# Kernel tuning notes

Hardware: AMD Instinct MI355X
Metric: run time of the kernel (lower is better)

The kernel has to match this reference:

```python
import jax, jax.numpy as jnp
import numpy as np

N_NODES = 100000
N_EDGES = 1600000
HIDDEN = 128


def setup_inputs() -> dict:
    key = jax.random.key(0)
    k1, k2, k3 = jax.random.split(key, 3)
    pos = jax.random.normal(k1, (N_NODES, 3), dtype=jnp.float32)
    edge_index = jax.random.randint(k2, (2, N_EDGES), 0, N_NODES, dtype=jnp.int64)
    vector_features = jax.random.normal(k3, (N_NODES, 3, HIDDEN), dtype=jnp.float32)
    return {"pos": pos, "edge_index": edge_index, "vector_features": vector_features}


def reference(pos, edge_index, vector_features):
    # pos: (N,3); edge_index: (2,E); vector_features: (N,3,H) (unused by original math)
    H = vector_features.shape[-1]
    n_nodes = pos.shape[0]
    row, col = edge_index[0], edge_index[1]

    edge_vec = pos[col] - pos[row]                                  # (E,3)
    edge_dist = jnp.linalg.norm(edge_vec, axis=-1, keepdims=True) + 1e-8
    unit_vec = edge_vec / edge_dist                                 # (E,3)

    # scatter-add of unit vectors to both endpoints
    direction_units = (jnp.zeros((n_nodes, 3), dtype=pos.dtype)
                       .at[row].add(unit_vec)
                       .at[col].add(-unit_vec))                     # (N,3)

    # sum over spatial dim of du*du -> squared norm, broadcast to hidden
    angular_info = jnp.broadcast_to(
        jnp.sum(direction_units * direction_units, axis=1, keepdims=True),
        (n_nodes, H))                                               # (N,H)

    # vectorized per-edge dihedral: project v_i, v_j off the edge direction
    v_i = direction_units[row]                                      # (E,3)
    v_j = direction_units[col]                                      # (E,3)
    dot_vi = jnp.sum(v_i * unit_vec, axis=-1, keepdims=True)
    dot_vj = jnp.sum(v_j * (-unit_vec), axis=-1, keepdims=True)
    w_ij = v_i - dot_vi * unit_vec
    w_ji = v_j - dot_vj * (-unit_vec)
    dihedral_val = jnp.sum(w_ij * w_ji, axis=-1, keepdims=True)     # (E,1)
    dihedral_info = jnp.broadcast_to(dihedral_val, (edge_index.shape[1], H))

    return (angular_info, dihedral_info, direction_units)
```

## Files before the change

kernel.cpp:

```cpp
#include <hip/hip_runtime.h>
#include <math.h>

#define N_NODES 100000
#define N_EDGES 1600000
#define HIDDEN 128

#define NBINS      256
#define BIN_NODES  391
#define BIN_CAP    16256
#define CUR_STRIDE 32
#define A_THREADS  1024
#define A_EPT      2
#define A_EPB      (A_THREADS * A_EPT)
#define A_BLOCKS   ((N_EDGES + A_EPB - 1) / A_EPB)
#define B_THREADS  1024

#define FP_SCALE   4194304.0f
#define FP_INV     (1.0f / 4194304.0f)


typedef float vfloat4 __attribute__((ext_vector_type(4)));

__global__ void zero_cursors_kernel(unsigned* __restrict__ cur) {
    cur[threadIdx.x * CUR_STRIDE] = 0u;
}

__global__ __launch_bounds__(A_THREADS) void bin_edges_kernel(
    const int* __restrict__ eidx,
    unsigned* __restrict__ cursors,
    unsigned* __restrict__ region)
{
    __shared__ unsigned cnt[NBINS];
    __shared__ unsigned base[NBINS];
    if (threadIdx.x < NBINS) cnt[threadIdx.x] = 0u;
    __syncthreads();

    const int e0 = blockIdx.x * A_EPB + threadIdx.x * 2;
    const bool valid = (e0 < N_EDGES);

    unsigned r[A_EPT], c[A_EPT], br[A_EPT], bc[A_EPT], orow[A_EPT], ocol[A_EPT];

    if (valid) {
        int2 rr = *reinterpret_cast<const int2*>(eidx + e0);
        int2 cc = *reinterpret_cast<const int2*>(eidx + N_EDGES + e0);
        r[0] = (unsigned)rr.x; r[1] = (unsigned)rr.y;
        c[0] = (unsigned)cc.x; c[1] = (unsigned)cc.y;
        #pragma unroll
        for (int k = 0; k < A_EPT; ++k) {
            br[k] = r[k] / BIN_NODES;
            bc[k] = c[k] / BIN_NODES;
            orow[k] = atomicAdd(&cnt[br[k]], 1u);
            ocol[k] = atomicAdd(&cnt[bc[k]], 1u);
        }
    }
    __syncthreads();

    if (threadIdx.x < NBINS)
        base[threadIdx.x] =
            atomicAdd(&cursors[threadIdx.x * CUR_STRIDE], cnt[threadIdx.x]);
    __syncthreads();

    if (valid) {
        #pragma unroll
        for (int k = 0; k < A_EPT; ++k) {
            region[br[k] * BIN_CAP + base[br[k]] + orow[k]] =
                ((r[k] - br[k] * BIN_NODES) << 17) | c[k];
            region[bc[k] * BIN_CAP + base[bc[k]] + ocol[k]] =
                ((c[k] - bc[k] * BIN_NODES) << 17) | r[k];
        }
    }
}

__device__ __forceinline__ void proc_rec(unsigned rec,
                                         const float* __restrict__ posLDS,
                                         const float* __restrict__ pos,
                                         int* __restrict__ acc) {
    unsigned other = rec & 0x1FFFFu;
    unsigned local = rec >> 17;
    float sx = posLDS[local * 3 + 0];
    float sy = posLDS[local * 3 + 1];
    float sz = posLDS[local * 3 + 2];
    float dx = pos[other * 3 + 0] - sx;
    float dy = pos[other * 3 + 1] - sy;
    float dz = pos[other * 3 + 2] - sz;
    float inv = 1.0f / (sqrtf(dx * dx + dy * dy + dz * dz) + 1e-8f);
    atomicAdd(&acc[local * 3 + 0], __float2int_rn(dx * inv * FP_SCALE));
    atomicAdd(&acc[local * 3 + 1], __float2int_rn(dy * inv * FP_SCALE));
    atomicAdd(&acc[local * 3 + 2], __float2int_rn(dz * inv * FP_SCALE));
}

__global__ __launch_bounds__(B_THREADS) void accumulate_kernel(
    const float* __restrict__ pos,
    const unsigned* __restrict__ cursors,
    const unsigned* __restrict__ region,
    float* __restrict__ du,
    float* __restrict__ ang)
{
    __shared__ int   acc[BIN_NODES * 3];
    __shared__ float posLDS[BIN_NODES * 3];
    const unsigned b = blockIdx.x;
    const unsigned nodebase = b * BIN_NODES;
    const unsigned nloc = min((unsigned)BIN_NODES,
                              (unsigned)(N_NODES - nodebase));

    for (int i = threadIdx.x; i < BIN_NODES * 3; i += B_THREADS) acc[i] = 0;
    for (unsigned i = threadIdx.x; i < nloc * 3; i += B_THREADS)
        posLDS[i] = pos[(size_t)nodebase * 3 + i];
    __syncthreads();

    const unsigned n = cursors[b * CUR_STRIDE];
    const unsigned* __restrict__ reg = region + (size_t)b * BIN_CAP;
    const unsigned n4 = n & ~3u;

    for (unsigned i = threadIdx.x * 4; i < n4; i += B_THREADS * 4) {
        uint4 rc = *reinterpret_cast<const uint4*>(reg + i);
        proc_rec(rc.x, posLDS, pos, acc);
        proc_rec(rc.y, posLDS, pos, acc);
        proc_rec(rc.z, posLDS, pos, acc);
        proc_rec(rc.w, posLDS, pos, acc);
    }
    for (unsigned i = n4 + threadIdx.x; i < n; i += B_THREADS)
        proc_rec(reg[i], posLDS, pos, acc);
    __syncthreads();

    for (unsigned i = threadIdx.x; i < nloc * 3; i += B_THREADS)
        du[(size_t)nodebase * 3 + i] = (float)acc[i] * FP_INV;

    for (unsigned j = threadIdx.x; j < nloc * 32; j += B_THREADS) {
        unsigned node = j >> 5, c4 = j & 31;
        float x = (float)acc[node * 3 + 0] * FP_INV;
        float y = (float)acc[node * 3 + 1] * FP_INV;
        float z = (float)acc[node * 3 + 2] * FP_INV;
        float a = x * x + y * y + z * z;
        vfloat4 v4 = {a, a, a, a};
        __builtin_nontemporal_store(v4,
            reinterpret_cast<vfloat4*>(ang + (size_t)(nodebase + node) * HIDDEN) + c4);
    }
}

__global__ __launch_bounds__(256) void dihedral_kernel(
    const float* __restrict__ pos,
    const int* __restrict__ eidx,
    const float* __restrict__ du,
    float* __restrict__ dih)
{
    __shared__ float vals[256];
    const int e0 = blockIdx.x * 256;
    const int e  = e0 + threadIdx.x;

    {
        int r = eidx[e];
        int c = eidx[N_EDGES + e];

        float dx = pos[c * 3 + 0] - pos[r * 3 + 0];
        float dy = pos[c * 3 + 1] - pos[r * 3 + 1];
        float dz = pos[c * 3 + 2] - pos[r * 3 + 2];
        float dist = sqrtf(dx * dx + dy * dy + dz * dz) + 1e-8f;
        float inv = 1.0f / dist;
        float ux = dx * inv, uy = dy * inv, uz = dz * inv;

        float vix = du[r * 3 + 0], viy = du[r * 3 + 1], viz = du[r * 3 + 2];
        float vjx = du[c * 3 + 0], vjy = du[c * 3 + 1], vjz = du[c * 3 + 2];

        float dvi = vix * ux + viy * uy + viz * uz;
        float dvj = -(vjx * ux + vjy * uy + vjz * uz);

        float wix = vix - dvi * ux;
        float wiy = viy - dvi * uy;
        float wiz = viz - dvi * uz;
        float wjx = vjx + dvj * ux;
        float wjy = vjy + dvj * uy;
        float wjz = vjz + dvj * uz;

        vals[threadIdx.x] = wix * wjx + wiy * wjy + wiz * wjz;
    }
    __syncthreads();

    vfloat4* out = reinterpret_cast<vfloat4*>(dih + (size_t)e0 * HIDDEN);
    #pragma unroll
    for (int it = 0; it < 32; ++it) {
        int i = it * 256 + threadIdx.x;
        float v = vals[i >> 5];
        vfloat4 v4 = {v, v, v, v};
        __builtin_nontemporal_store(v4, out + i);
    }
}

__global__ void zero_du_kernel(float* __restrict__ du, int n) {
    int i = blockIdx.x * blockDim.x + threadIdx.x;
    if (i < n) du[i] = 0.0f;
}

__global__ void edge_scatter_kernel(const float* __restrict__ pos,
                                    const int* __restrict__ eidx,
                                    float* __restrict__ du) {
    int e = blockIdx.x * blockDim.x + threadIdx.x;
    if (e >= N_EDGES) return;
    int r = eidx[e];
    int c = eidx[N_EDGES + e];
    float dx = pos[c * 3 + 0] - pos[r * 3 + 0];
    float dy = pos[c * 3 + 1] - pos[r * 3 + 1];
    float dz = pos[c * 3 + 2] - pos[r * 3 + 2];
    float inv = 1.0f / (sqrtf(dx * dx + dy * dy + dz * dz) + 1e-8f);
    float ux = dx * inv, uy = dy * inv, uz = dz * inv;
    unsafeAtomicAdd(&du[r * 3 + 0],  ux);
    unsafeAtomicAdd(&du[r * 3 + 1],  uy);
    unsafeAtomicAdd(&du[r * 3 + 2],  uz);
    unsafeAtomicAdd(&du[c * 3 + 0], -ux);
    unsafeAtomicAdd(&du[c * 3 + 1], -uy);
    unsafeAtomicAdd(&du[c * 3 + 2], -uz);
}

__global__ void angular_kernel(const float* __restrict__ du,
                               float* __restrict__ ang) {
    int gid = blockIdx.x * blockDim.x + threadIdx.x;
    int node = gid >> 5;
    int c4   = gid & 31;
    float x = du[node * 3 + 0];
    float y = du[node * 3 + 1];
    float z = du[node * 3 + 2];
    float a = x * x + y * y + z * z;
    vfloat4 v4 = {a, a, a, a};
    __builtin_nontemporal_store(v4,
        reinterpret_cast<vfloat4*>(ang + (size_t)node * HIDDEN) + c4);
}

extern "C" void kernel_launch(void* const* d_in, const int* in_sizes, int n_in,
                              void* d_out, int out_size, void* d_ws, size_t ws_size,
                              hipStream_t stream) {
    const float* pos  = (const float*)d_in[0];
    const int*   eidx = (const int*)d_in[1];

    float* out = (float*)d_out;
    float* ang = out;
    float* dih = out + (size_t)N_NODES * HIDDEN;
    float* du  = dih + (size_t)N_EDGES * HIDDEN;

    const size_t curBytes = (size_t)NBINS * CUR_STRIDE * sizeof(unsigned);
    const size_t need = curBytes + (size_t)NBINS * BIN_CAP * sizeof(unsigned);

    if (ws_size >= need) {
        unsigned* cursors = (unsigned*)d_ws;
        unsigned* region  = (unsigned*)d_ws + NBINS * CUR_STRIDE;

        zero_cursors_kernel<<<1, NBINS, 0, stream>>>(cursors);
        bin_edges_kernel<<<A_BLOCKS, A_THREADS, 0, stream>>>(eidx, cursors, region);
        accumulate_kernel<<<NBINS, B_THREADS, 0, stream>>>(pos, cursors,
                                                           region, du, ang);
    } else {
        zero_du_kernel<<<(N_NODES * 3 + 255) / 256, 256, 0, stream>>>(du, N_NODES * 3);
        edge_scatter_kernel<<<(N_EDGES + 255) / 256, 256, 0, stream>>>(pos, eidx, du);
        angular_kernel<<<(N_NODES * 32) / 256, 256, 0, stream>>>(du, ang);
    }

    dihedral_kernel<<<N_EDGES / 256, 256, 0, stream>>>(pos, eidx, du, dih);
}
```

Measured before the change: 217.8 us.

## Pad positions to float4 and process more edges per binning thread

A prep kernel now zeroes the bin cursors and also copies positions into a padded float4 array. The accumulate kernel then fetches each neighbor position with one 16-byte gather instead of three scalar loads. The binning kernel processes 8 edges per thread instead of 2, which reduces the number of blocks and the global cursor atomics. BIN_CAP is cut to 14336, which leaves less headroom per bin for random edge distributions and could overflow if a bin gets unusually many records.

```diff
diff --git a/kernel.cpp b/kernel.cpp
--- a/kernel.cpp
+++ b/kernel.cpp
@@ -7,10 +7,10 @@
 
 #define NBINS      256
 #define BIN_NODES  391
-#define BIN_CAP    16256
+#define BIN_CAP    14336
 #define CUR_STRIDE 32
 #define A_THREADS  1024
-#define A_EPT      2
+#define A_EPT      8
 #define A_EPB      (A_THREADS * A_EPT)
 #define A_BLOCKS   ((N_EDGES + A_EPB - 1) / A_EPB)
 #define B_THREADS  1024
@@ -21,8 +21,17 @@
 
 typedef float vfloat4 __attribute__((ext_vector_type(4)));
 
-__global__ void zero_cursors_kernel(unsigned* __restrict__ cur) {
-    cur[threadIdx.x * CUR_STRIDE] = 0u;
+__global__ __launch_bounds__(256) void prep_kernel(
+    const float* __restrict__ pos,
+    unsigned* __restrict__ cursors,
+    float4* __restrict__ pos4)
+{
+    int gid = blockIdx.x * 256 + threadIdx.x;
+    if (gid < NBINS) cursors[gid * CUR_STRIDE] = 0u;
+    if (gid < N_NODES) {
+        pos4[gid] = make_float4(pos[gid * 3 + 0], pos[gid * 3 + 1],
+                                pos[gid * 3 + 2], 0.0f);
+    }
 }
 
 __global__ __launch_bounds__(A_THREADS) void bin_edges_kernel(
@@ -35,18 +44,26 @@
     if (threadIdx.x < NBINS) cnt[threadIdx.x] = 0u;
     __syncthreads();
 
-    const int e0 = blockIdx.x * A_EPB + threadIdx.x * 2;
-    const bool valid = (e0 < N_EDGES);
-
+    const int eb = blockIdx.x * A_EPB + threadIdx.x * 2;
+
+    bool     val[A_EPT];
     unsigned r[A_EPT], c[A_EPT], br[A_EPT], bc[A_EPT], orow[A_EPT], ocol[A_EPT];
 
-    if (valid) {
-        int2 rr = *reinterpret_cast<const int2*>(eidx + e0);
-        int2 cc = *reinterpret_cast<const int2*>(eidx + N_EDGES + e0);
-        r[0] = (unsigned)rr.x; r[1] = (unsigned)rr.y;
-        c[0] = (unsigned)cc.x; c[1] = (unsigned)cc.y;
-        #pragma unroll
-        for (int k = 0; k < A_EPT; ++k) {
+    #pragma unroll
+    for (int k = 0; k < A_EPT; k += 2) {
+        int e = eb + k * A_THREADS;
+        bool v = (e < N_EDGES);
+        val[k] = v; val[k + 1] = v;
+        if (v) {
+            int2 rr = *reinterpret_cast<const int2*>(eidx + e);
+            int2 cc = *reinterpret_cast<const int2*>(eidx + N_EDGES + e);
+            r[k] = (unsigned)rr.x; r[k + 1] = (unsigned)rr.y;
+            c[k] = (unsigned)cc.x; c[k + 1] = (unsigned)cc.y;
+        }
+    }
+    #pragma unroll
+    for (int k = 0; k < A_EPT; ++k) {
+        if (val[k]) {
             br[k] = r[k] / BIN_NODES;
             bc[k] = c[k] / BIN_NODES;
             orow[k] = atomicAdd(&cnt[br[k]], 1u);
@@ -60,9 +77,9 @@
             atomicAdd(&cursors[threadIdx.x * CUR_STRIDE], cnt[threadIdx.x]);
     __syncthreads();
 
-    if (valid) {
-        #pragma unroll
-        for (int k = 0; k < A_EPT; ++k) {
+    #pragma unroll
+    for (int k = 0; k < A_EPT; ++k) {
+        if (val[k]) {
             region[br[k] * BIN_CAP + base[br[k]] + orow[k]] =
                 ((r[k] - br[k] * BIN_NODES) << 17) | c[k];
             region[bc[k] * BIN_CAP + base[bc[k]] + ocol[k]] =
@@ -72,17 +89,16 @@
 }
 
 __device__ __forceinline__ void proc_rec(unsigned rec,
-                                         const float* __restrict__ posLDS,
-                                         const float* __restrict__ pos,
+                                         const float4* __restrict__ posLDS4,
+                                         const float4* __restrict__ pos4,
                                          int* __restrict__ acc) {
     unsigned other = rec & 0x1FFFFu;
     unsigned local = rec >> 17;
-    float sx = posLDS[local * 3 + 0];
-    float sy = posLDS[local * 3 + 1];
-    float sz = posLDS[local * 3 + 2];
-    float dx = pos[other * 3 + 0] - sx;
-    float dy = pos[other * 3 + 1] - sy;
-    float dz = pos[other * 3 + 2] - sz;
+    float4 s = posLDS4[local];
+    float4 p = pos4[other];
+    float dx = p.x - s.x;
+    float dy = p.y - s.y;
+    float dz = p.z - s.z;
     float inv = 1.0f / (sqrtf(dx * dx + dy * dy + dz * dz) + 1e-8f);
     atomicAdd(&acc[local * 3 + 0], __float2int_rn(dx * inv * FP_SCALE));
     atomicAdd(&acc[local * 3 + 1], __float2int_rn(dy * inv * FP_SCALE));
@@ -90,22 +106,22 @@
 }
 
 __global__ __launch_bounds__(B_THREADS) void accumulate_kernel(
-    const float* __restrict__ pos,
+    const float4* __restrict__ pos4,
     const unsigned* __restrict__ cursors,
     const unsigned* __restrict__ region,
     float* __restrict__ du,
     float* __restrict__ ang)
 {
-    __shared__ int   acc[BIN_NODES * 3];
-    __shared__ float posLDS[BIN_NODES * 3];
+    __shared__ int    acc[BIN_NODES * 3];
+    __shared__ float4 posLDS4[BIN_NODES];
     const unsigned b = blockIdx.x;
     const unsigned nodebase = b * BIN_NODES;
     const unsigned nloc = min((unsigned)BIN_NODES,
                               (unsigned)(N_NODES - nodebase));
 
     for (int i = threadIdx.x; i < BIN_NODES * 3; i += B_THREADS) acc[i] = 0;
-    for (unsigned i = threadIdx.x; i < nloc * 3; i += B_THREADS)
-        posLDS[i] = pos[(size_t)nodebase * 3 + i];
+    for (unsigned i = threadIdx.x; i < nloc; i += B_THREADS)
+        posLDS4[i] = pos4[nodebase + i];
     __syncthreads();
 
     const unsigned n = cursors[b * CUR_STRIDE];
@@ -114,13 +130,13 @@
 
     for (unsigned i = threadIdx.x * 4; i < n4; i += B_THREADS * 4) {
         uint4 rc = *reinterpret_cast<const uint4*>(reg + i);
-        proc_rec(rc.x, posLDS, pos, acc);
-        proc_rec(rc.y, posLDS, pos, acc);
-        proc_rec(rc.z, posLDS, pos, acc);
-        proc_rec(rc.w, posLDS, pos, acc);
+        proc_rec(rc.x, posLDS4, pos4, acc);
+        proc_rec(rc.y, posLDS4, pos4, acc);
+        proc_rec(rc.z, posLDS4, pos4, acc);
+        proc_rec(rc.w, posLDS4, pos4, acc);
     }
     for (unsigned i = n4 + threadIdx.x; i < n; i += B_THREADS)
-        proc_rec(reg[i], posLDS, pos, acc);
+        proc_rec(reg[i], posLDS4, pos4, acc);
     __syncthreads();
 
     for (unsigned i = threadIdx.x; i < nloc * 3; i += B_THREADS)
@@ -236,16 +252,19 @@
     float* dih = out + (size_t)N_NODES * HIDDEN;
     float* du  = dih + (size_t)N_EDGES * HIDDEN;
 
-    const size_t curBytes = (size_t)NBINS * CUR_STRIDE * sizeof(unsigned);
-    const size_t need = curBytes + (size_t)NBINS * BIN_CAP * sizeof(unsigned);
+    const size_t curWords = (size_t)NBINS * CUR_STRIDE;
+    const size_t regWords = (size_t)NBINS * BIN_CAP;
+    const size_t need = (curWords + regWords) * sizeof(unsigned)
+                      + (size_t)(N_NODES + 64) * sizeof(float4);
 
     if (ws_size >= need) {
         unsigned* cursors = (unsigned*)d_ws;
-        unsigned* region  = (unsigned*)d_ws + NBINS * CUR_STRIDE;
-
-        zero_cursors_kernel<<<1, NBINS, 0, stream>>>(cursors);
+        unsigned* region  = cursors + curWords;
+        float4*   pos4    = (float4*)(region + regWords);
+
+        prep_kernel<<<(N_NODES + 255) / 256, 256, 0, stream>>>(pos, cursors, pos4);
         bin_edges_kernel<<<A_BLOCKS, A_THREADS, 0, stream>>>(eidx, cursors, region);
-        accumulate_kernel<<<NBINS, B_THREADS, 0, stream>>>(pos, cursors,
+        accumulate_kernel<<<NBINS, B_THREADS, 0, stream>>>(pos4, cursors,
                                                            region, du, ang);
     } else {
         zero_du_kernel<<<(N_NODES * 3 + 255) / 256, 256, 0, stream>>>(du, N_NODES * 3);
```

Result: no change. 213.6 us (-1.9%).
